# Performance work log

Measured on AMD Instinct MI355X. Metric: run time of the kernel, lower is better.

Reference implementation:

```python
import math
import jax, jax.numpy as jnp
import numpy as np

HIDDEN = 2880
HEAD_DIM = 64
N_HEADS = 64
N_KV = 8
Q_MULT = N_HEADS // N_KV  # 8
QKV_DIM = HEAD_DIM * (N_HEADS + 2 * N_KV)  # 5120
SLIDING_WINDOW = 128
SM_SCALE = 1.0 / math.sqrt(HEAD_DIM)
ROPE_BASE = 150000.0
ROPE_SCALING = 32.0
INIT_CTX = 4096
NTK_ALPHA = 1.0
NTK_BETA = 32.0
EPS = 1e-5
N_TOKENS = 1536


def rope_tables(n):
    # YaRN-style inv_freq mixing (scaling_factor > 1 branch)
    d = HEAD_DIM
    freq = ROPE_BASE ** (jnp.arange(0, d, 2, dtype=jnp.float32) / d)
    concentration = 0.1 * math.log(ROPE_SCALING) + 1.0
    d_half = d / 2
    low = d_half * math.log(INIT_CTX / (NTK_BETA * 2 * math.pi)) / math.log(ROPE_BASE)
    high = d_half * math.log(INIT_CTX / (NTK_ALPHA * 2 * math.pi)) / math.log(ROPE_BASE)
    interpolation = 1.0 / (ROPE_SCALING * freq)
    extrapolation = 1.0 / freq
    ramp = (jnp.arange(d_half, dtype=jnp.float32) - low) / (high - low)
    mask = 1.0 - jnp.clip(ramp, 0.0, 1.0)
    inv_freq = interpolation * (1.0 - mask) + extrapolation * mask
    t = jnp.arange(n, dtype=jnp.float32)
    freqs = t[:, None] * inv_freq[None, :]  # (n, d/2)
    return jnp.cos(freqs) * concentration, jnp.sin(freqs) * concentration


def apply_rotary(x, cos, sin):
    # x: (n, H, d); cos/sin: (n, d/2)
    c = cos[:, None, :]
    s = sin[:, None, :]
    x1, x2 = jnp.split(x, 2, axis=-1)
    return jnp.concatenate([x1 * c - x2 * s, x2 * c + x1 * s], axis=-1)


def setup_inputs() -> dict:
    key = jax.random.key(0)
    ks = jax.random.split(key, 7)
    x = jax.random.normal(ks[0], (N_TOKENS, HIDDEN), dtype=jnp.float32)
    norm_scale = jnp.ones((HIDDEN,), dtype=jnp.float32)
    qkv_w = jax.random.normal(ks[1], (QKV_DIM, HIDDEN), dtype=jnp.float32) * 0.02
    qkv_b = jax.random.normal(ks[2], (QKV_DIM,), dtype=jnp.float32) * 0.02
    out_w = jax.random.normal(ks[3], (HIDDEN, HEAD_DIM * N_HEADS), dtype=jnp.float32) * 0.02
    out_b = jax.random.normal(ks[4], (HIDDEN,), dtype=jnp.float32) * 0.02
    sinks = jax.random.normal(ks[5], (N_HEADS,), dtype=jnp.float32)
    return {"x": x, "norm_scale": norm_scale, "qkv_w": qkv_w, "qkv_b": qkv_b,
            "out_w": out_w, "out_b": out_b, "sinks": sinks}


def reference(x, norm_scale, qkv_w, qkv_b, out_w, out_b, sinks):
    n = x.shape[0]
    # RMSNorm (fp32)
    t = x * jax.lax.rsqrt(jnp.mean(x * x, axis=-1, keepdims=True) + EPS) * norm_scale
    # fused QKV projection
    qkv = t @ qkv_w.T + qkv_b  # (n, QKV_DIM)
    q = qkv[:, : N_HEADS * HEAD_DIM].reshape(n, N_KV, Q_MULT, HEAD_DIM)
    k = qkv[:, N_HEADS * HEAD_DIM : (N_HEADS + N_KV) * HEAD_DIM].reshape(n, N_KV, HEAD_DIM)
    v = qkv[:, (N_HEADS + N_KV) * HEAD_DIM :].reshape(n, N_KV, HEAD_DIM)
    # RoPE
    cos, sin = rope_tables(n)
    q = apply_rotary(q.reshape(n, N_HEADS, HEAD_DIM), cos, sin).reshape(n, N_KV, Q_MULT, HEAD_DIM)
    k = apply_rotary(k, cos, sin)
    # attention with causal + sliding-window mask and sink logits
    i = jnp.arange(n)[:, None]
    j = jnp.arange(n)[None, :]
    allowed = (j <= i) & (j > i - SLIDING_WINDOW)
    mask = jnp.where(allowed, 0.0, -jnp.inf).astype(jnp.float32)  # (q, k)
    scores = jnp.einsum('qhmd,khd->hmqk', q, k) * SM_SCALE + mask[None, None, :, :]
    s = sinks.reshape(N_KV, Q_MULT, 1, 1)
    s = jnp.broadcast_to(s, (N_KV, Q_MULT, n, 1))
    logits = jnp.concatenate([scores, s], axis=-1)
    w = jax.nn.softmax(logits, axis=-1)[..., :-1]  # drop sink column
    attn = jnp.einsum('hmqk,khd->qhmd', w, v).reshape(n, N_HEADS * HEAD_DIM)
    # output projection + residual
    return x + attn @ out_w.T + out_b
```

## Files before the change

kernel.cpp:

```cpp
#include <hip/hip_runtime.h>

typedef __attribute__((ext_vector_type(8))) short bf16x8;
typedef __attribute__((ext_vector_type(4))) float f32x4;

#define HIDDEN 2880
#define QKV_DIM 5120
#define NH 64
#define NKV 8
#define HD 64
#define ATT_DIM 4096
#define WINDOW 128
#define SM_SCALE 0.125f

__device__ __forceinline__ ushort f2bf(float f) {
  union { float f; unsigned u; } a; a.f = f;
  unsigned r = a.u + 0x7fffu + ((a.u >> 16) & 1u);
  return (ushort)(r >> 16);
}

__device__ __forceinline__ void gload_lds16(const void* g, void* l) {
  __builtin_amdgcn_global_load_lds((const __attribute__((address_space(1))) void*)g,
                                   (__attribute__((address_space(3))) void*)l, 16, 0, 0);
}

__global__ __launch_bounds__(256) void cvt_f32_bf16(const float* __restrict__ in,
                                                    ushort* __restrict__ out, int n4) {
  int i = blockIdx.x * blockDim.x + threadIdx.x;
  int stride = gridDim.x * blockDim.x;
  for (; i < n4; i += stride) {
    float4 v = ((const float4*)in)[i];
    ushort4 o = { f2bf(v.x), f2bf(v.y), f2bf(v.z), f2bf(v.w) };
    ((ushort4*)out)[i] = o;
  }
}

__global__ __launch_bounds__(256) void rmsnorm_bf16(const float* __restrict__ x,
                                                    const float* __restrict__ scale,
                                                    ushort* __restrict__ t) {
  int row = blockIdx.x;
  int tid = threadIdx.x;
  const float4* xr = (const float4*)(x + (size_t)row * HIDDEN);
  float4 a0 = xr[tid];
  float4 a1 = xr[tid + 256];
  bool has2 = tid < 208;
  float4 a2 = has2 ? xr[tid + 512] : float4{0.f, 0.f, 0.f, 0.f};
  float ss = a0.x*a0.x + a0.y*a0.y + a0.z*a0.z + a0.w*a0.w
           + a1.x*a1.x + a1.y*a1.y + a1.z*a1.z + a1.w*a1.w
           + a2.x*a2.x + a2.y*a2.y + a2.z*a2.z + a2.w*a2.w;
  for (int m = 1; m < 64; m <<= 1) ss += __shfl_xor(ss, m, 64);
  __shared__ float red[4];
  if ((tid & 63) == 0) red[tid >> 6] = ss;
  __syncthreads();
  ss = red[0] + red[1] + red[2] + red[3];
  float r = rsqrtf(ss / (float)HIDDEN + 1e-5f);
  ushort4* tr = (ushort4*)(t + (size_t)row * HIDDEN);
  const float4* sc4 = (const float4*)scale;
  {
    float4 s = sc4[tid];
    ushort4 o = { f2bf(a0.x*r*s.x), f2bf(a0.y*r*s.y), f2bf(a0.z*r*s.z), f2bf(a0.w*r*s.w) };
    tr[tid] = o;
  }
  {
    float4 s = sc4[tid + 256];
    ushort4 o = { f2bf(a1.x*r*s.x), f2bf(a1.y*r*s.y), f2bf(a1.z*r*s.z), f2bf(a1.w*r*s.w) };
    tr[tid + 256] = o;
  }
  if (has2) {
    float4 s = sc4[tid + 512];
    ushort4 o = { f2bf(a2.x*r*s.x), f2bf(a2.y*r*s.y), f2bf(a2.z*r*s.z), f2bf(a2.w*r*s.w) };
    tr[tid + 512] = o;
  }
}

template <int MASK_N>
__global__ __launch_bounds__(512)
void gemm_8p(const ushort* __restrict__ A, const ushort* __restrict__ B,
             float* __restrict__ P, int M, int N, int K, int NSK) {
  __shared__ __align__(16) ushort Al[2][256 * 64];
  __shared__ __align__(16) ushort Bl[2][256 * 64];
  const int tid = threadIdx.x;
  const int wave = tid >> 6, lane = tid & 63;
  const int l15 = lane & 15, hi = lane >> 4;

  int nwg = gridDim.x, orig = blockIdx.x;
  int q8 = nwg >> 3, r8 = nwg & 7, xcd = orig & 7, seq = orig >> 3;
  int swz = (xcd < r8 ? xcd * (q8 + 1) : r8 * (q8 + 1) + (xcd - r8) * q8) + seq;
  int nm = M >> 8;
  int bm = swz % nm, bn = swz / nm;
  const int row0 = bm * 256, col0 = bn * 256;
  const int sk = blockIdx.y;
  const int NTtot = K >> 6;
  const int tt0 = sk * NTtot / NSK, tt1 = (sk + 1) * NTtot / NSK;
  float* Pp = P + (size_t)sk * M * N;

  const int wrow = (wave >> 2) * 128;
  const int wcol = (wave & 3) * 64;
  const int srow = lane >> 3;
  const int schunk = (lane & 7) ^ srow;

  f32x4 acc[8][4] = {};

  auto stageA = [&](int t, int r) {
    int row = row0 + r * 64 + wave * 8 + srow;
    gload_lds16(A + (size_t)row * K + (t << 6) + schunk * 8,
                &Al[t & 1][(r * 64 + wave * 8) * 64]);
  };
  auto stageB = [&](int t, int r) {
    int brow = col0 + r * 64 + wave * 8 + srow;
    if (MASK_N) { if (brow > N - 1) brow = N - 1; }
    gload_lds16(B + (size_t)brow * K + (t << 6) + schunk * 8,
                &Bl[t & 1][(r * 64 + wave * 8) * 64]);
  };
  auto stageAll = [&](int t) {
#pragma unroll
    for (int r = 0; r < 4; ++r) { stageA(t, r); stageB(t, r); }
  };
  auto LDA = [&](bf16x8 (&dst)[4][2], int mh, const char* base) {
#pragma unroll
    for (int mt = 0; mt < 4; ++mt)
#pragma unroll
      for (int ks = 0; ks < 2; ++ks) {
        int rr = wrow + mh * 64 + mt * 16 + l15;
        int off = (rr * 128 + ks * 64 + hi * 16) ^ ((rr & 7) << 4);
        dst[mt][ks] = *(const bf16x8*)(base + off);
      }
  };
  auto LDB = [&](bf16x8 (&dst)[2][2], int nh, const char* base) {
#pragma unroll
    for (int nt = 0; nt < 2; ++nt)
#pragma unroll
      for (int ks = 0; ks < 2; ++ks) {
        int rr = wcol + nh * 32 + nt * 16 + l15;
        int off = (rr * 128 + ks * 64 + hi * 16) ^ ((rr & 7) << 4);
        dst[nt][ks] = *(const bf16x8*)(base + off);
      }
  };
  auto MMA = [&](bf16x8 (&a)[4][2], bf16x8 (&b)[2][2], int mh, int nh) {
    __builtin_amdgcn_s_setprio(1);
#pragma unroll
    for (int ks = 0; ks < 2; ++ks)
#pragma unroll
      for (int nt = 0; nt < 2; ++nt)
#pragma unroll
        for (int mt = 0; mt < 4; ++mt)
          acc[mh * 4 + mt][nh * 2 + nt] = __builtin_amdgcn_mfma_f32_16x16x32_bf16(
              a[mt][ks], b[nt][ks], acc[mh * 4 + mt][nh * 2 + nt], 0, 0, 0);
    __builtin_amdgcn_s_setprio(0);
  };

  stageAll(tt0);
  bool two = (tt1 - tt0 > 1);
  if (two) {
    stageAll(tt0 + 1);
    asm volatile("s_waitcnt vmcnt(8)" ::: "memory");
  } else {
    asm volatile("s_waitcnt vmcnt(0)" ::: "memory");
  }
  __builtin_amdgcn_s_barrier();

  for (int t = tt0; t < tt1; ++t) {
    const char* Ab = (const char*)&Al[t & 1][0];
    const char* Bb = (const char*)&Bl[t & 1][0];
    bool pre = (t + 2 < tt1);
    bf16x8 afr[4][2], bf0[2][2], bf1[2][2];
    LDA(afr, 0, Ab);
    LDB(bf0, 0, Bb);
    __builtin_amdgcn_s_barrier();
    MMA(afr, bf0, 0, 0);
    __builtin_amdgcn_s_barrier();
    LDB(bf1, 1, Bb);
    if (pre) { stageA(t + 2, 0); stageA(t + 2, 2); }
    __builtin_amdgcn_s_barrier();
    MMA(afr, bf1, 0, 1);
    __builtin_amdgcn_s_barrier();
    LDA(afr, 1, Ab);
    if (pre) { stageB(t + 2, 0); stageB(t + 2, 1); stageB(t + 2, 2); stageB(t + 2, 3); }
    __builtin_amdgcn_s_barrier();
    MMA(afr, bf1, 1, 1);
    __builtin_amdgcn_s_barrier();
    if (pre) { stageA(t + 2, 1); stageA(t + 2, 3); }
    __builtin_amdgcn_s_barrier();
    MMA(afr, bf0, 1, 0);
    if (pre) asm volatile("s_waitcnt vmcnt(8)" ::: "memory");
    else     asm volatile("s_waitcnt vmcnt(0)" ::: "memory");
    __builtin_amdgcn_s_barrier();
  }

#pragma unroll
  for (int mtg = 0; mtg < 8; ++mtg) {
#pragma unroll
    for (int nt = 0; nt < 4; ++nt) {
#pragma unroll
      for (int rr = 0; rr < 4; ++rr) {
        int row = row0 + wrow + mtg * 16 + (hi << 2) + rr;
        int col = col0 + wcol + nt * 16 + l15;
        if (!MASK_N || col < N) Pp[(size_t)row * N + col] = acc[mtg][nt][rr];
      }
    }
  }
}

__global__ __launch_bounds__(256)
void reduce_out(const float* __restrict__ x, const float* __restrict__ b,
                const float* __restrict__ p, int nsk, size_t stride,
                float* __restrict__ out, int n4, int N) {
  int i = blockIdx.x * blockDim.x + threadIdx.x;
  if (i >= n4) return;
  float4 v = ((const float4*)x)[i];
  int col = (i * 4) % N;
  float4 bb = *(const float4*)(b + col);
  v.x += bb.x; v.y += bb.y; v.z += bb.z; v.w += bb.w;
  for (int s = 0; s < nsk; ++s) {
    float4 pv = *(const float4*)(p + s * stride + (size_t)i * 4);
    v.x += pv.x; v.y += pv.y; v.z += pv.z; v.w += pv.w;
  }
  ((float4*)out)[i] = v;
}

__global__ __launch_bounds__(256)
void rope_split(const float* __restrict__ p, size_t stride, const float* __restrict__ qkvb,
                ushort* __restrict__ qb, ushort* __restrict__ kb, ushort* __restrict__ vb) {
  int tok = blockIdx.x;
  int tid = threadIdx.x;
  __shared__ float cs[32], sn[32];
  if (tid < 32) {
    float d = (float)tid;
    float freq = powf(150000.0f, d / 32.0f);
    float conc = 0.1f * logf(32.0f) + 1.0f;
    float lg = logf(150000.0f);
    float low = 32.0f * logf(4096.0f / (32.0f * 6.2831853f)) / lg;
    float high = 32.0f * logf(4096.0f / 6.2831853f) / lg;
    float ramp = (d - low) / (high - low);
    float cl = fminf(fmaxf(ramp, 0.0f), 1.0f);
    float mask = 1.0f - cl;
    float inv_freq = (1.0f - mask) / (32.0f * freq) + mask / freq;
    float fr = (float)tok * inv_freq;
    cs[tid] = cosf(fr) * conc;
    sn[tid] = sinf(fr) * conc;
  }
  __syncthreads();
  const float* r0 = p + (size_t)tok * QKV_DIM;
  const float* r1 = r0 + stride;
  auto ld = [&](int c) { return r0[c] + r1[c] + qkvb[c]; };
#pragma unroll
  for (int it = 0; it < 8; ++it) {
    int pp = tid + it * 256;
    int hd = pp >> 5, d = pp & 31;
    float x1 = ld(hd * 64 + d), x2 = ld(hd * 64 + d + 32);
    float c = cs[d], s = sn[d];
    size_t o = ((size_t)tok * NH + hd) * HD + d;
    qb[o] = f2bf(x1 * c - x2 * s);
    qb[o + 32] = f2bf(x2 * c + x1 * s);
  }
  {
    int pp = tid;
    int hd = pp >> 5, d = pp & 31;
    float x1 = ld(4096 + hd * 64 + d), x2 = ld(4096 + hd * 64 + d + 32);
    float c = cs[d], s = sn[d];
    size_t o = ((size_t)tok * NKV + hd) * HD + d;
    kb[o] = f2bf(x1 * c - x2 * s);
    kb[o + 32] = f2bf(x2 * c + x1 * s);
  }
#pragma unroll
  for (int it = 0; it < 2; ++it) {
    int pp = tid + it * 256;
    vb[(size_t)tok * (NKV * HD) + pp] = f2bf(ld(4608 + pp));
  }
}

__global__ __launch_bounds__(512)
void attn_fused(const ushort* __restrict__ qb, const ushort* __restrict__ kb,
                const ushort* __restrict__ vb, const float* __restrict__ sinks,
                ushort* __restrict__ attn, int n) {
  __shared__ __align__(16) ushort Kl[160 * 64];
  __shared__ __align__(16) ushort Vt[64 * 168];
  __shared__ __align__(16) ushort Pl[8][32 * 40];
  int tid = threadIdx.x;
  int wave = tid >> 6, lane = tid & 63;
  int qstart = blockIdx.x * 32;
  int kv = blockIdx.y;
  int head = kv * 8 + wave;
  int key0 = qstart - 128;

  for (int i = 0; i < 3; ++i) {
    int rowb = i * 64 + wave * 8;
    if (rowb < 160) {
      int r = rowb + (lane >> 3);
      int gj = key0 + r; if (gj < 0) gj = 0;
      int chunk = (lane & 7) ^ (lane >> 3);
      gload_lds16(kb + ((size_t)gj * NKV + kv) * HD + chunk * 8, Kl + rowb * 64);
    }
  }
  for (int e = tid; e < 160 * 16; e += 512) {
    int j = e >> 4, d4 = (e & 15) << 2;
    int gj = key0 + j; if (gj < 0) gj = 0;
    ushort4 v = *(const ushort4*)(vb + ((size_t)gj * NKV + kv) * HD + d4);
    Vt[(d4 + 0) * 168 + j] = v.x;
    Vt[(d4 + 1) * 168 + j] = v.y;
    Vt[(d4 + 2) * 168 + j] = v.z;
    Vt[(d4 + 3) * 168 + j] = v.w;
  }
  bf16x8 qf[2][2];
#pragma unroll
  for (int mt = 0; mt < 2; ++mt)
#pragma unroll
    for (int ks = 0; ks < 2; ++ks) {
      int r = qstart + mt * 16 + (lane & 15);
      int kk = ks * 32 + ((lane >> 4) << 3);
      qf[mt][ks] = *(const bf16x8*)(qb + ((size_t)r * NH + head) * HD + kk);
    }
  __syncthreads();

  f32x4 s[2][10] = {};
#pragma unroll
  for (int nt = 0; nt < 10; ++nt) {
#pragma unroll
    for (int ks = 0; ks < 2; ++ks) {
      int r = nt * 16 + (lane & 15);
      int off = (r * 128 + (ks * 32 + ((lane >> 4) << 3)) * 2) ^ ((r & 7) << 4);
      bf16x8 kf = *(const bf16x8*)((const char*)Kl + off);
      s[0][nt] = __builtin_amdgcn_mfma_f32_16x16x32_bf16(qf[0][ks], kf, s[0][nt], 0, 0, 0);
      s[1][nt] = __builtin_amdgcn_mfma_f32_16x16x32_bf16(qf[1][ks], kf, s[1][nt], 0, 0, 0);
    }
  }

  float lrow[2][4];
  float snk = sinks[head];
#pragma unroll
  for (int mt = 0; mt < 2; ++mt) {
#pragma unroll
    for (int r = 0; r < 4; ++r) {
      int i = qstart + mt * 16 + ((lane >> 4) << 2) + r;
      float mx = -1e30f;
#pragma unroll
      for (int nt = 0; nt < 10; ++nt) {
        int j = key0 + nt * 16 + (lane & 15);
        bool ok = (j >= 0) && (j <= i) && (j > i - WINDOW);
        float val = ok ? s[mt][nt][r] * SM_SCALE : -1e30f;
        s[mt][nt][r] = val;
        mx = fmaxf(mx, val);
      }
      mx = fmaxf(mx, __shfl_xor(mx, 1, 64));
      mx = fmaxf(mx, __shfl_xor(mx, 2, 64));
      mx = fmaxf(mx, __shfl_xor(mx, 4, 64));
      mx = fmaxf(mx, __shfl_xor(mx, 8, 64));
      mx = fmaxf(mx, snk);
      float sum = 0.f;
#pragma unroll
      for (int nt = 0; nt < 10; ++nt) {
        float pv = expf(s[mt][nt][r] - mx);
        s[mt][nt][r] = pv;
        sum += pv;
      }
      sum += __shfl_xor(sum, 1, 64);
      sum += __shfl_xor(sum, 2, 64);
      sum += __shfl_xor(sum, 4, 64);
      sum += __shfl_xor(sum, 8, 64);
      sum += expf(snk - mx);
      lrow[mt][r] = sum;
    }
  }

  f32x4 o[2][4] = {};
#pragma unroll
  for (int kc = 0; kc < 5; ++kc) {
    __syncthreads();
#pragma unroll
    for (int mt = 0; mt < 2; ++mt)
#pragma unroll
      for (int t2 = 0; t2 < 2; ++t2) {
        int nt = kc * 2 + t2;
#pragma unroll
        for (int r = 0; r < 4; ++r) {
          int prow = mt * 16 + ((lane >> 4) << 2) + r;
          int pcol = t2 * 16 + (lane & 15);
          Pl[wave][prow * 40 + pcol] = f2bf(s[mt][nt][r]);
        }
      }
    __syncthreads();
    bf16x8 pa[2];
#pragma unroll
    for (int mt = 0; mt < 2; ++mt) {
      int r = mt * 16 + (lane & 15);
      pa[mt] = *(const bf16x8*)(&Pl[wave][r * 40 + ((lane >> 4) << 3)]);
    }
#pragma unroll
    for (int nt = 0; nt < 4; ++nt) {
      int d = nt * 16 + (lane & 15);
      int kk = kc * 32 + ((lane >> 4) << 3);
      bf16x8 vf = *(const bf16x8*)(&Vt[d * 168 + kk]);
      o[0][nt] = __builtin_amdgcn_mfma_f32_16x16x32_bf16(pa[0], vf, o[0][nt], 0, 0, 0);
      o[1][nt] = __builtin_amdgcn_mfma_f32_16x16x32_bf16(pa[1], vf, o[1][nt], 0, 0, 0);
    }
  }

#pragma unroll
  for (int mt = 0; mt < 2; ++mt)
#pragma unroll
    for (int nt = 0; nt < 4; ++nt)
#pragma unroll
      for (int r = 0; r < 4; ++r) {
        int row = qstart + mt * 16 + ((lane >> 4) << 2) + r;
        int d = nt * 16 + (lane & 15);
        float val = o[mt][nt][r] / lrow[mt][r];
        attn[((size_t)row * NH + head) * HD + d] = f2bf(val);
      }
}

extern "C" void kernel_launch(void* const* d_in, const int* in_sizes, int n_in,
                              void* d_out, int out_size, void* d_ws, size_t ws_size,
                              hipStream_t stream) {
  const float* x      = (const float*)d_in[0];
  const float* nscale = (const float*)d_in[1];
  const float* qkv_w  = (const float*)d_in[2];
  const float* qkv_b  = (const float*)d_in[3];
  const float* out_w  = (const float*)d_in[4];
  const float* out_b  = (const float*)d_in[5];
  const float* sinks  = (const float*)d_in[6];
  float* out = (float*)d_out;
  int n = in_sizes[0] / HIDDEN;

  char* ws = (char*)d_ws;
  size_t off = 0;
  auto alloc = [&](size_t bytes) {
    char* p = ws + off;
    off += (bytes + 255) & ~(size_t)255;
    return p;
  };
  ushort* t_bf    = (ushort*)alloc((size_t)n * HIDDEN * 2);
  ushort* qkvw_bf = (ushort*)alloc((size_t)QKV_DIM * HIDDEN * 2);
  ushort* outw_bf = (ushort*)alloc((size_t)HIDDEN * ATT_DIM * 2);
  ushort* q_bf    = (ushort*)alloc((size_t)n * NH * HD * 2);
  ushort* k_bf    = (ushort*)alloc((size_t)n * NKV * HD * 2);
  ushort* v_bf    = (ushort*)alloc((size_t)n * NKV * HD * 2);
  ushort* attn    = (ushort*)alloc((size_t)n * ATT_DIM * 2);
  size_t qkv_ps = (size_t)n * QKV_DIM;
  size_t out_ps = (size_t)n * HIDDEN;
  size_t pelems = 2 * qkv_ps > 3 * out_ps ? 2 * qkv_ps : 3 * out_ps;
  float* partials = (float*)alloc(pelems * 4);

  cvt_f32_bf16<<<2048, 256, 0, stream>>>(qkv_w, qkvw_bf, QKV_DIM * HIDDEN / 4);
  cvt_f32_bf16<<<2048, 256, 0, stream>>>(out_w, outw_bf, HIDDEN * ATT_DIM / 4);
  rmsnorm_bf16<<<n, 256, 0, stream>>>(x, nscale, t_bf);
  gemm_8p<0><<<dim3((n / 256) * (QKV_DIM / 256), 2), 512, 0, stream>>>(
      t_bf, qkvw_bf, partials, n, QKV_DIM, HIDDEN, 2);
  rope_split<<<n, 256, 0, stream>>>(partials, qkv_ps, qkv_b, q_bf, k_bf, v_bf);
  attn_fused<<<dim3(n / 32, NKV), 512, 0, stream>>>(q_bf, k_bf, v_bf, sinks, attn, n);
  gemm_8p<1><<<dim3((n / 256) * 12, 3), 512, 0, stream>>>(
      attn, outw_bf, partials, n, HIDDEN, ATT_DIM, 3);
  reduce_out<<<(n * HIDDEN / 4 + 255) / 256, 256, 0, stream>>>(
      x, out_b, partials, 3, out_ps, out, n * HIDDEN / 4, HIDDEN);
}
```

Baseline: 193.1 us.

## Halve attention query tile per block and drop intra-wave P barriers

The attention kernel now processes 16 query rows per block instead of 32, doubling the grid so more blocks can run at once, and shrinks the per-wave P buffer. The two __syncthreads around the per-wave P staging are removed, since each wave only reads its own LDS slice. expf is replaced by __expf. In exchange, each block still stages 160 keys and values and computes 10 score tiles for only 16 queries, so K/V load and QK work per query roughly doubles.

```diff
diff --git a/kernel.cpp b/kernel.cpp
--- a/kernel.cpp
+++ b/kernel.cpp
@@ -274,10 +274,11 @@
                 ushort* __restrict__ attn, int n) {
   __shared__ __align__(16) ushort Kl[160 * 64];
   __shared__ __align__(16) ushort Vt[64 * 168];
-  __shared__ __align__(16) ushort Pl[8][32 * 40];
+  __shared__ __align__(16) ushort Pl[8][16 * 40];
   int tid = threadIdx.x;
   int wave = tid >> 6, lane = tid & 63;
-  int qstart = blockIdx.x * 32;
+  int l15 = lane & 15, hi = lane >> 4;
+  int qstart = blockIdx.x * 16;
   int kv = blockIdx.y;
   int head = kv * 8 + wave;
   int key0 = qstart - 128;
@@ -300,111 +301,90 @@
     Vt[(d4 + 2) * 168 + j] = v.z;
     Vt[(d4 + 3) * 168 + j] = v.w;
   }
-  bf16x8 qf[2][2];
-#pragma unroll
-  for (int mt = 0; mt < 2; ++mt)
+  bf16x8 qf[2];
+#pragma unroll
+  for (int ks = 0; ks < 2; ++ks) {
+    int r = qstart + l15;
+    int kk = ks * 32 + hi * 8;
+    qf[ks] = *(const bf16x8*)(qb + ((size_t)r * NH + head) * HD + kk);
+  }
+  __syncthreads();
+
+  f32x4 s[10] = {};
+#pragma unroll
+  for (int nt = 0; nt < 10; ++nt) {
 #pragma unroll
     for (int ks = 0; ks < 2; ++ks) {
-      int r = qstart + mt * 16 + (lane & 15);
-      int kk = ks * 32 + ((lane >> 4) << 3);
-      qf[mt][ks] = *(const bf16x8*)(qb + ((size_t)r * NH + head) * HD + kk);
-    }
-  __syncthreads();
-
-  f32x4 s[2][10] = {};
-#pragma unroll
-  for (int nt = 0; nt < 10; ++nt) {
-#pragma unroll
-    for (int ks = 0; ks < 2; ++ks) {
-      int r = nt * 16 + (lane & 15);
-      int off = (r * 128 + (ks * 32 + ((lane >> 4) << 3)) * 2) ^ ((r & 7) << 4);
+      int r = nt * 16 + l15;
+      int off = (r * 128 + (ks * 32 + hi * 8) * 2) ^ ((r & 7) << 4);
       bf16x8 kf = *(const bf16x8*)((const char*)Kl + off);
-      s[0][nt] = __builtin_amdgcn_mfma_f32_16x16x32_bf16(qf[0][ks], kf, s[0][nt], 0, 0, 0);
-      s[1][nt] = __builtin_amdgcn_mfma_f32_16x16x32_bf16(qf[1][ks], kf, s[1][nt], 0, 0, 0);
-    }
-  }
-
-  float lrow[2][4];
+      s[nt] = __builtin_amdgcn_mfma_f32_16x16x32_bf16(qf[ks], kf, s[nt], 0, 0, 0);
+    }
+  }
+
+  float lrow[4];
   float snk = sinks[head];
 #pragma unroll
-  for (int mt = 0; mt < 2; ++mt) {
+  for (int r = 0; r < 4; ++r) {
+    int i = qstart + hi * 4 + r;
+    float mx = -1e30f;
+#pragma unroll
+    for (int nt = 0; nt < 10; ++nt) {
+      int j = key0 + nt * 16 + l15;
+      bool ok = (j >= 0) && (j <= i) && (j > i - WINDOW);
+      float val = ok ? s[nt][r] * SM_SCALE : -1e30f;
+      s[nt][r] = val;
+      mx = fmaxf(mx, val);
+    }
+    mx = fmaxf(mx, __shfl_xor(mx, 1, 64));
+    mx = fmaxf(mx, __shfl_xor(mx, 2, 64));
+    mx = fmaxf(mx, __shfl_xor(mx, 4, 64));
+    mx = fmaxf(mx, __shfl_xor(mx, 8, 64));
+    mx = fmaxf(mx, snk);
+    float sum = 0.f;
+#pragma unroll
+    for (int nt = 0; nt < 10; ++nt) {
+      float pv = __expf(s[nt][r] - mx);
+      s[nt][r] = pv;
+      sum += pv;
+    }
+    sum += __shfl_xor(sum, 1, 64);
+    sum += __shfl_xor(sum, 2, 64);
+    sum += __shfl_xor(sum, 4, 64);
+    sum += __shfl_xor(sum, 8, 64);
+    sum += __expf(snk - mx);
+    lrow[r] = sum;
+  }
+
+  f32x4 o[4] = {};
+#pragma unroll
+  for (int kc = 0; kc < 5; ++kc) {
+#pragma unroll
+    for (int t2 = 0; t2 < 2; ++t2) {
+      int nt = kc * 2 + t2;
+#pragma unroll
+      for (int r = 0; r < 4; ++r)
+        Pl[wave][(hi * 4 + r) * 40 + t2 * 16 + l15] = f2bf(s[nt][r]);
+    }
+    bf16x8 pa = *(const bf16x8*)(&Pl[wave][l15 * 40 + hi * 8]);
+#pragma unroll
+    for (int nt = 0; nt < 4; ++nt) {
+      int d = nt * 16 + l15;
+      int kk = kc * 32 + hi * 8;
+      bf16x8 vf = *(const bf16x8*)(&Vt[d * 168 + kk]);
+      o[nt] = __builtin_amdgcn_mfma_f32_16x16x32_bf16(pa, vf, o[nt], 0, 0, 0);
+    }
+  }
+
+#pragma unroll
+  for (int nt = 0; nt < 4; ++nt)
 #pragma unroll
     for (int r = 0; r < 4; ++r) {
-      int i = qstart + mt * 16 + ((lane >> 4) << 2) + r;
-      float mx = -1e30f;
-#pragma unroll
-      for (int nt = 0; nt < 10; ++nt) {
-        int j = key0 + nt * 16 + (lane & 15);
-        bool ok = (j >= 0) && (j <= i) && (j > i - WINDOW);
-        float val = ok ? s[mt][nt][r] * SM_SCALE : -1e30f;
-        s[mt][nt][r] = val;
-        mx = fmaxf(mx, val);
-      }
-      mx = fmaxf(mx, __shfl_xor(mx, 1, 64));
-      mx = fmaxf(mx, __shfl_xor(mx, 2, 64));
-      mx = fmaxf(mx, __shfl_xor(mx, 4, 64));
-      mx = fmaxf(mx, __shfl_xor(mx, 8, 64));
-      mx = fmaxf(mx, snk);
-      float sum = 0.f;
-#pragma unroll
-      for (int nt = 0; nt < 10; ++nt) {
-        float pv = expf(s[mt][nt][r] - mx);
-        s[mt][nt][r] = pv;
-        sum += pv;
-      }
-      sum += __shfl_xor(sum, 1, 64);
-      sum += __shfl_xor(sum, 2, 64);
-      sum += __shfl_xor(sum, 4, 64);
-      sum += __shfl_xor(sum, 8, 64);
-      sum += expf(snk - mx);
-      lrow[mt][r] = sum;
-    }
-  }
-
-  f32x4 o[2][4] = {};
-#pragma unroll
-  for (int kc = 0; kc < 5; ++kc) {
-    __syncthreads();
-#pragma unroll
-    for (int mt = 0; mt < 2; ++mt)
-#pragma unroll
-      for (int t2 = 0; t2 < 2; ++t2) {
-        int nt = kc * 2 + t2;
-#pragma unroll
-        for (int r = 0; r < 4; ++r) {
-          int prow = mt * 16 + ((lane >> 4) << 2) + r;
-          int pcol = t2 * 16 + (lane & 15);
-          Pl[wave][prow * 40 + pcol] = f2bf(s[mt][nt][r]);
-        }
-      }
-    __syncthreads();
-    bf16x8 pa[2];
-#pragma unroll
-    for (int mt = 0; mt < 2; ++mt) {
-      int r = mt * 16 + (lane & 15);
-      pa[mt] = *(const bf16x8*)(&Pl[wave][r * 40 + ((lane >> 4) << 3)]);
-    }
-#pragma unroll
-    for (int nt = 0; nt < 4; ++nt) {
-      int d = nt * 16 + (lane & 15);
-      int kk = kc * 32 + ((lane >> 4) << 3);
-      bf16x8 vf = *(const bf16x8*)(&Vt[d * 168 + kk]);
-      o[0][nt] = __builtin_amdgcn_mfma_f32_16x16x32_bf16(pa[0], vf, o[0][nt], 0, 0, 0);
-      o[1][nt] = __builtin_amdgcn_mfma_f32_16x16x32_bf16(pa[1], vf, o[1][nt], 0, 0, 0);
-    }
-  }
-
-#pragma unroll
-  for (int mt = 0; mt < 2; ++mt)
-#pragma unroll
-    for (int nt = 0; nt < 4; ++nt)
-#pragma unroll
-      for (int r = 0; r < 4; ++r) {
-        int row = qstart + mt * 16 + ((lane >> 4) << 2) + r;
-        int d = nt * 16 + (lane & 15);
-        float val = o[mt][nt][r] / lrow[mt][r];
-        attn[((size_t)row * NH + head) * HD + d] = f2bf(val);
-      }
+      int row = qstart + hi * 4 + r;
+      int d = nt * 16 + l15;
+      float val = o[nt][r] / lrow[r];
+      attn[((size_t)row * NH + head) * HD + d] = f2bf(val);
+    }
 }
 
 extern "C" void kernel_launch(void* const* d_in, const int* in_sizes, int n_in,
@@ -445,7 +425,7 @@
   gemm_8p<0><<<dim3((n / 256) * (QKV_DIM / 256), 2), 512, 0, stream>>>(
       t_bf, qkvw_bf, partials, n, QKV_DIM, HIDDEN, 2);
   rope_split<<<n, 256, 0, stream>>>(partials, qkv_ps, qkv_b, q_bf, k_bf, v_bf);
-  attn_fused<<<dim3(n / 32, NKV), 512, 0, stream>>>(q_bf, k_bf, v_bf, sinks, attn, n);
+  attn_fused<<<dim3(n / 16, NKV), 512, 0, stream>>>(q_bf, k_bf, v_bf, sinks, attn, n);
   gemm_8p<1><<<dim3((n / 256) * 12, 3), 512, 0, stream>>>(
       attn, outw_bf, partials, n, HIDDEN, ATT_DIM, 3);
   reduce_out<<<(n * HIDDEN / 4 + 255) / 256, 256, 0, stream>>>(
```

Result: faster. 180.6 us (-6.4%).
